# Optimization experiments

Measured on AMD Instinct MI355X. Metric: run time of the kernel, lower is better.

## Reference

```python
import jax, jax.numpy as jnp
from jax import lax
import numpy as np

N_FEATURE = 128
EDGE = 12          # int(sqrt(128) + 1)
BATCH = 131072


def maxpool2(x):
    # 2x2 max pool, stride 2, NCHW
    return lax.reduce_window(x, -jnp.inf, lax.max,
                             (1, 1, 2, 2), (1, 1, 2, 2), 'VALID')


def conv3x3(x, w, b):
    # 3x3 conv, padding=1, NCHW / OIHW
    y = lax.conv_general_dilated(x, w, window_strides=(1, 1),
                                 padding=((1, 1), (1, 1)),
                                 dimension_numbers=('NCHW', 'OIHW', 'NCHW'))
    return y + b[None, :, None, None]


def setup_inputs() -> dict:
    key = jax.random.key(0)
    ks = jax.random.split(key, 9)
    x = jax.random.normal(ks[0], (BATCH, N_FEATURE), dtype=jnp.float32)
    conv1_w = jax.random.normal(ks[1], (3, 1, 3, 3), dtype=jnp.float32) * 0.1
    conv1_b = jnp.zeros((3,), dtype=jnp.float32)
    conv2_w = jax.random.normal(ks[2], (6, 3, 3, 3), dtype=jnp.float32) * 0.1
    conv2_b = jnp.zeros((6,), dtype=jnp.float32)
    fc1_w = jax.random.normal(ks[3], (128, 54), dtype=jnp.float32) * 0.1
    fc1_b = jnp.zeros((128,), dtype=jnp.float32)
    out_w = jax.random.normal(ks[4], (N_FEATURE, 128), dtype=jnp.float32) * 0.1
    out_b = jnp.zeros((N_FEATURE,), dtype=jnp.float32)
    return {"x": x, "conv1_w": conv1_w, "conv1_b": conv1_b,
            "conv2_w": conv2_w, "conv2_b": conv2_b,
            "fc1_w": fc1_w, "fc1_b": fc1_b,
            "out_w": out_w, "out_b": out_b}


def reference(x, conv1_w, conv1_b, conv2_w, conv2_b, fc1_w, fc1_b, out_w, out_b):
    num = x.shape[0]
    n = x.shape[1]                       # 128
    pad = EDGE * EDGE - n                # 16 trailing zeros
    # vectorized transto3D: row-major fill of edge x edge grid, zero-padded tail
    g = jnp.pad(x, ((0, 0), (0, pad))).reshape(num, 1, EDGE, EDGE)
    h = jax.nn.relu(maxpool2(conv3x3(g, conv1_w, conv1_b)))      # [num,3,6,6]
    h = jax.nn.relu(maxpool2(conv3x3(h, conv2_w, conv2_b)))      # [num,6,3,3]
    h = h.reshape(num, 54)
    h = jax.nn.relu(h @ fc1_w.T + fc1_b)                         # [num,128]
    return h @ out_w.T + out_b                                   # [num,128]
```

## Files before the change

### kernel.cpp

```cpp
#include <hip/hip_runtime.h>

typedef unsigned int uint;
typedef unsigned short ushort;

using bf16x8 = __attribute__((ext_vector_type(8))) short;
using f32x4  = __attribute__((ext_vector_type(4))) float;

__device__ __forceinline__ float b2f(ushort u) {
  union { uint i; float f; } v; v.i = ((uint)u) << 16; return v.f;
}
__device__ __forceinline__ ushort f2b(float f) {
  union { float f; uint i; } v; v.f = f;
  uint r = (v.i + 0x7fffu + ((v.i >> 16) & 1u)) >> 16;
  return (ushort)r;
}
__device__ __forceinline__ bf16x8 ldfrag(const ushort* p) {
  union { uint4 u; bf16x8 v; } x; x.u = *(const uint4*)p; return x.v;
}
__device__ __forceinline__ bf16x8 pack8(const float4 a, const float4 b) {
  union { uint4 u; bf16x8 v; } x;
  x.u.x = (uint)f2b(a.x) | ((uint)f2b(a.y) << 16);
  x.u.y = (uint)f2b(a.z) | ((uint)f2b(a.w) << 16);
  x.u.z = (uint)f2b(b.x) | ((uint)f2b(b.y) << 16);
  x.u.w = (uint)f2b(b.z) | ((uint)f2b(b.w) << 16);
  return x.v;
}

__global__ __launch_bounds__(256, 1) void conv_kernel(
    const float* __restrict__ x,
    const float* __restrict__ w1g, const float* __restrict__ b1g,
    const float* __restrict__ w2g, const float* __restrict__ b2g,
    ushort* __restrict__ h2ws) {
  const int s = blockIdx.x * 256 + threadIdx.x;
  const float* xs = x + (size_t)s * 128;

  float xv[128];
#pragma unroll
  for (int i = 0; i < 32; ++i) {
    const float4 v = ((const float4*)xs)[i];
    xv[4 * i + 0] = v.x; xv[4 * i + 1] = v.y;
    xv[4 * i + 2] = v.z; xv[4 * i + 3] = v.w;
  }
#pragma unroll
  for (int i = 0; i < 128; ++i) asm volatile("" : "+v"(xv[i]));

  float w1[3][9], b1[3];
#pragma unroll
  for (int c = 0; c < 3; ++c) {
    b1[c] = b1g[c];
#pragma unroll
    for (int q = 0; q < 9; ++q) w1[c][q] = w1g[c * 9 + q];
  }

  float h1[3][6][6];
#pragma unroll
  for (int pr = 0; pr < 6; ++pr)
#pragma unroll
    for (int pc = 0; pc < 6; ++pc)
#pragma unroll
      for (int ch = 0; ch < 3; ++ch) {
        float m = -3.0e38f;
#pragma unroll
        for (int dr = 0; dr < 2; ++dr)
#pragma unroll
          for (int dc = 0; dc < 2; ++dc) {
            float a = 0.f;
#pragma unroll
            for (int ky = 0; ky < 3; ++ky)
#pragma unroll
              for (int kx = 0; kx < 3; ++kx) {
                const int r = 2 * pr + dr + ky - 1;
                const int c = 2 * pc + dc + kx - 1;
                if (r >= 0 && r < 12 && c >= 0 && c < 12 && (12 * r + c) < 128)
                  a = fmaf(w1[ch][ky * 3 + kx], xv[12 * r + c], a);
              }
            m = fmaxf(m, a);
          }
        h1[ch][pr][pc] = fmaxf(m + b1[ch], 0.f);
      }

  float h2[54];
#pragma unroll
  for (int o = 0; o < 6; ++o) {
    float w2[27];
#pragma unroll
    for (int q = 0; q < 27; ++q) w2[q] = w2g[o * 27 + q];
    const float bo = b2g[o];
#pragma unroll
    for (int qr = 0; qr < 3; ++qr)
#pragma unroll
      for (int qc = 0; qc < 3; ++qc) {
        float m = -3.0e38f;
#pragma unroll
        for (int dr = 0; dr < 2; ++dr)
#pragma unroll
          for (int dc = 0; dc < 2; ++dc) {
            float a = 0.f;
#pragma unroll
            for (int i = 0; i < 3; ++i)
#pragma unroll
              for (int ky = 0; ky < 3; ++ky)
#pragma unroll
                for (int kx = 0; kx < 3; ++kx) {
                  const int yy = 2 * qr + dr + ky - 1;
                  const int xx = 2 * qc + dc + kx - 1;
                  if (yy >= 0 && yy < 6 && xx >= 0 && xx < 6)
                    a = fmaf(w2[i * 9 + ky * 3 + kx], h1[i][yy][xx], a);
                }
            m = fmaxf(m, a);
          }
        h2[o * 9 + qr * 3 + qc] = fmaxf(m + bo, 0.f);
      }
  }

  uint pk[32];
#pragma unroll
  for (int q = 0; q < 27; ++q)
    pk[q] = (uint)f2b(h2[2 * q]) | ((uint)f2b(h2[2 * q + 1]) << 16);
#pragma unroll
  for (int q = 27; q < 32; ++q) pk[q] = 0u;
  uint4* dst = (uint4*)(h2ws + (size_t)s * 64);
#pragma unroll
  for (int i = 0; i < 8; ++i) {
    uint4 v; v.x = pk[4 * i]; v.y = pk[4 * i + 1];
    v.z = pk[4 * i + 2]; v.w = pk[4 * i + 3];
    dst[i] = v;
  }
}

__global__ __launch_bounds__(256, 3) void fc_kernel(
    const ushort* __restrict__ h2ws,
    const float* __restrict__ fc1w, const float* __restrict__ fc1b,
    const float* __restrict__ outw, const float* __restrict__ outb,
    float* __restrict__ out) {
  __shared__ __align__(16) ushort w1s[128][72];
  __shared__ __align__(16) ushort tA[128][132];
  __shared__ __align__(16) float fb1[128];
  __shared__ __align__(16) float ob[128];

  const int t = threadIdx.x;
  const int s0 = blockIdx.x * 128;
  const int lane = t & 63, wv = t >> 6;
  const int quad = lane >> 4, lm = lane & 15;

  bf16x8 bh[2][8];
#pragma unroll
  for (int st = 0; st < 8; ++st) {
    const ushort* rp = h2ws + (size_t)(s0 + 16 * st + lm) * 64 + quad * 8;
    bh[0][st] = ldfrag(rp);
    bh[1][st] = ldfrag(rp + 32);
  }

  if (t < 128) { fb1[t] = fc1b[t]; ob[t] = outb[t]; }

#pragma unroll
  for (int i = 0; i < 27; ++i) {
    const int f = t + 256 * i;
    const int n = f / 54, k = f - 54 * n;
    w1s[n][k] = f2b(fc1w[f]);
  }
  if (t < 128) {
    uint* p = (uint*)&w1s[t][54];
#pragma unroll
    for (int q = 0; q < 5; ++q) p[q] = 0u;
  }
  __syncthreads();

  f32x4 acc[2][8];
#pragma unroll
  for (int mt = 0; mt < 2; ++mt)
#pragma unroll
    for (int st = 0; st < 8; ++st) acc[mt][st] = (f32x4){0.f, 0.f, 0.f, 0.f};

#pragma unroll
  for (int kk = 0; kk < 2; ++kk) {
    const int ko = kk * 32 + quad * 8;
    bf16x8 aw[2];
#pragma unroll
    for (int mt = 0; mt < 2; ++mt)
      aw[mt] = ldfrag(&w1s[32 * wv + 16 * mt + lm][ko]);
#pragma unroll
    for (int mt = 0; mt < 2; ++mt)
#pragma unroll
      for (int st = 0; st < 8; ++st)
        acc[mt][st] = __builtin_amdgcn_mfma_f32_16x16x32_bf16(
            aw[mt], bh[kk][st], acc[mt][st], 0, 0, 0);
  }

#pragma unroll
  for (int mt = 0; mt < 2; ++mt) {
    const int jb = 32 * wv + 16 * mt + quad * 4;
    const float4 bj = *(const float4*)&fb1[jb];
#pragma unroll
    for (int st = 0; st < 8; ++st) {
      const int sR = 16 * st + lm;
      const float v0 = fmaxf(acc[mt][st][0] + bj.x, 0.f);
      const float v1 = fmaxf(acc[mt][st][1] + bj.y, 0.f);
      const float v2 = fmaxf(acc[mt][st][2] + bj.z, 0.f);
      const float v3 = fmaxf(acc[mt][st][3] + bj.w, 0.f);
      uint2 pv;
      pv.x = (uint)f2b(v0) | ((uint)f2b(v1) << 16);
      pv.y = (uint)f2b(v2) | ((uint)f2b(v3) << 16);
      *(uint2*)&tA[sR][jb] = pv;
    }
  }
  __syncthreads();

  f32x4 acc2[2][8];
#pragma unroll
  for (int mt = 0; mt < 2; ++mt)
#pragma unroll
    for (int st = 0; st < 8; ++st) acc2[mt][st] = (f32x4){0.f, 0.f, 0.f, 0.f};

#pragma unroll
  for (int kk = 0; kk < 4; ++kk) {
    const int ko = kk * 32 + quad * 8;
    bf16x8 ao[2], bt[8];
#pragma unroll
    for (int mt = 0; mt < 2; ++mt) {
      const float* rp = outw + (size_t)(32 * wv + 16 * mt + lm) * 128 + ko;
      const float4 v0 = *(const float4*)rp;
      const float4 v1 = *(const float4*)(rp + 4);
      ao[mt] = pack8(v0, v1);
    }
#pragma unroll
    for (int st = 0; st < 8; ++st)
      bt[st] = ldfrag(&tA[16 * st + lm][ko]);
#pragma unroll
    for (int mt = 0; mt < 2; ++mt)
#pragma unroll
      for (int st = 0; st < 8; ++st)
        acc2[mt][st] = __builtin_amdgcn_mfma_f32_16x16x32_bf16(
            ao[mt], bt[st], acc2[mt][st], 0, 0, 0);
  }

#pragma unroll
  for (int mt = 0; mt < 2; ++mt) {
    const int obase = 32 * wv + 16 * mt + quad * 4;
    const float4 b4 = *(const float4*)&ob[obase];
#pragma unroll
    for (int st = 0; st < 8; ++st) {
      const int srow = s0 + 16 * st + lm;
      float4 o4;
      o4.x = acc2[mt][st][0] + b4.x;
      o4.y = acc2[mt][st][1] + b4.y;
      o4.z = acc2[mt][st][2] + b4.z;
      o4.w = acc2[mt][st][3] + b4.w;
      *(float4*)&out[(size_t)srow * 128 + obase] = o4;
    }
  }
}

extern "C" void kernel_launch(void* const* d_in, const int* in_sizes, int n_in,
                              void* d_out, int out_size, void* d_ws, size_t ws_size,
                              hipStream_t stream) {
  const float* x    = (const float*)d_in[0];
  const float* w1   = (const float*)d_in[1];
  const float* b1   = (const float*)d_in[2];
  const float* w2   = (const float*)d_in[3];
  const float* b2   = (const float*)d_in[4];
  const float* fc1w = (const float*)d_in[5];
  const float* fc1b = (const float*)d_in[6];
  const float* outw = (const float*)d_in[7];
  const float* outb = (const float*)d_in[8];
  float* outp = (float*)d_out;
  ushort* ws  = (ushort*)d_ws;

  const int N = in_sizes[0] / 128;

  conv_kernel<<<N / 256, 256, 0, stream>>>(x, w1, b1, w2, b2, ws);
  fc_kernel<<<N / 128, 256, 0, stream>>>(ws, fc1w, fc1b, outw, outb, outp);
}
```

Before: 180.8 us.

## Split conv per sample across three waves by output row band

The conv kernel now gives each sample to three threads, one per pooled conv2 output row. Each thread loads only the input rows it needs and computes only the h1 rows its band requires. Results are staged in shared memory and written to the workspace with coalesced 32-bit stores. This cuts per-thread register pressure and raises occupancy relative to the one-thread-per-sample design at launch bound 1, at the cost of recomputing the overlapping h1 rows and reading some input rows redundantly.

```diff
diff --git a/kernel.cpp b/kernel.cpp
--- a/kernel.cpp
+++ b/kernel.cpp
@@ -26,23 +26,25 @@
   return x.v;
 }
 
-__global__ __launch_bounds__(256, 1) void conv_kernel(
-    const float* __restrict__ x,
+template <int Q>
+__device__ __forceinline__ void conv_sample(
+    const float* __restrict__ xs,
     const float* __restrict__ w1g, const float* __restrict__ b1g,
     const float* __restrict__ w2g, const float* __restrict__ b2g,
-    ushort* __restrict__ h2ws) {
-  const int s = blockIdx.x * 256 + threadIdx.x;
-  const float* xs = x + (size_t)s * 128;
+    ushort* __restrict__ strow) {
+  constexpr int HRLO = (Q == 0) ? 0 : (Q == 1) ? 1 : 3;
+  constexpr int HRHI = (Q == 0) ? 2 : (Q == 1) ? 4 : 5;
+  constexpr int NR = HRHI - HRLO + 1;
+  constexpr int F4LO = (Q == 0) ? 0 : (Q == 1) ? 3 : 15;
+  constexpr int F4HI = (Q == 0) ? 20 : 31;
 
   float xv[128];
 #pragma unroll
-  for (int i = 0; i < 32; ++i) {
+  for (int i = F4LO; i <= F4HI; ++i) {
     const float4 v = ((const float4*)xs)[i];
     xv[4 * i + 0] = v.x; xv[4 * i + 1] = v.y;
     xv[4 * i + 2] = v.z; xv[4 * i + 3] = v.w;
   }
-#pragma unroll
-  for (int i = 0; i < 128; ++i) asm volatile("" : "+v"(xv[i]));
 
   float w1[3][9], b1[3];
 #pragma unroll
@@ -52,9 +54,10 @@
     for (int q = 0; q < 9; ++q) w1[c][q] = w1g[c * 9 + q];
   }
 
-  float h1[3][6][6];
-#pragma unroll
-  for (int pr = 0; pr < 6; ++pr)
+  float h1[3][NR][6];
+#pragma unroll
+  for (int ri = 0; ri < NR; ++ri) {
+    const int hr = HRLO + ri;
 #pragma unroll
     for (int pc = 0; pc < 6; ++pc)
 #pragma unroll
@@ -69,17 +72,17 @@
             for (int ky = 0; ky < 3; ++ky)
 #pragma unroll
               for (int kx = 0; kx < 3; ++kx) {
-                const int r = 2 * pr + dr + ky - 1;
+                const int r = 2 * hr + dr + ky - 1;
                 const int c = 2 * pc + dc + kx - 1;
                 if (r >= 0 && r < 12 && c >= 0 && c < 12 && (12 * r + c) < 128)
                   a = fmaf(w1[ch][ky * 3 + kx], xv[12 * r + c], a);
               }
             m = fmaxf(m, a);
           }
-        h1[ch][pr][pc] = fmaxf(m + b1[ch], 0.f);
+        h1[ch][ri][pc] = fmaxf(m + b1[ch], 0.f);
       }
-
-  float h2[54];
+  }
+
 #pragma unroll
   for (int o = 0; o < 6; ++o) {
     float w2[27];
@@ -87,48 +90,71 @@
     for (int q = 0; q < 27; ++q) w2[q] = w2g[o * 27 + q];
     const float bo = b2g[o];
 #pragma unroll
-    for (int qr = 0; qr < 3; ++qr)
-#pragma unroll
-      for (int qc = 0; qc < 3; ++qc) {
-        float m = -3.0e38f;
-#pragma unroll
-        for (int dr = 0; dr < 2; ++dr)
-#pragma unroll
-          for (int dc = 0; dc < 2; ++dc) {
-            float a = 0.f;
-#pragma unroll
-            for (int i = 0; i < 3; ++i)
-#pragma unroll
-              for (int ky = 0; ky < 3; ++ky)
-#pragma unroll
-                for (int kx = 0; kx < 3; ++kx) {
-                  const int yy = 2 * qr + dr + ky - 1;
-                  const int xx = 2 * qc + dc + kx - 1;
-                  if (yy >= 0 && yy < 6 && xx >= 0 && xx < 6)
-                    a = fmaf(w2[i * 9 + ky * 3 + kx], h1[i][yy][xx], a);
-                }
-            m = fmaxf(m, a);
-          }
-        h2[o * 9 + qr * 3 + qc] = fmaxf(m + bo, 0.f);
-      }
-  }
-
-  uint pk[32];
-#pragma unroll
-  for (int q = 0; q < 27; ++q)
-    pk[q] = (uint)f2b(h2[2 * q]) | ((uint)f2b(h2[2 * q + 1]) << 16);
-#pragma unroll
-  for (int q = 27; q < 32; ++q) pk[q] = 0u;
-  uint4* dst = (uint4*)(h2ws + (size_t)s * 64);
-#pragma unroll
-  for (int i = 0; i < 8; ++i) {
-    uint4 v; v.x = pk[4 * i]; v.y = pk[4 * i + 1];
-    v.z = pk[4 * i + 2]; v.w = pk[4 * i + 3];
-    dst[i] = v;
-  }
-}
-
-__global__ __launch_bounds__(256, 3) void fc_kernel(
+    for (int qc = 0; qc < 3; ++qc) {
+      float m = -3.0e38f;
+#pragma unroll
+      for (int dr = 0; dr < 2; ++dr)
+#pragma unroll
+        for (int dc = 0; dc < 2; ++dc) {
+          float a = 0.f;
+#pragma unroll
+          for (int i = 0; i < 3; ++i)
+#pragma unroll
+            for (int ky = 0; ky < 3; ++ky)
+#pragma unroll
+              for (int kx = 0; kx < 3; ++kx) {
+                const int yy = 2 * Q + dr + ky - 1;
+                const int xx = 2 * qc + dc + kx - 1;
+                if (yy >= HRLO && yy <= HRHI && xx >= 0 && xx < 6)
+                  a = fmaf(w2[i * 9 + ky * 3 + kx], h1[i][yy - HRLO][xx], a);
+              }
+          m = fmaxf(m, a);
+        }
+      strow[o * 9 + Q * 3 + qc] = f2b(fmaxf(m + bo, 0.f));
+    }
+  }
+  if (Q == 2) {
+    uint* p = (uint*)(strow + 54);
+#pragma unroll
+    for (int q = 0; q < 5; ++q) p[q] = 0u;
+  }
+}
+
+__global__ __launch_bounds__(384, 6) void conv_kernel_r7(
+    const float* __restrict__ x,
+    const float* __restrict__ w1g, const float* __restrict__ b1g,
+    const float* __restrict__ w2g, const float* __restrict__ b2g,
+    ushort* __restrict__ h2ws) {
+  __shared__ ushort h2st[128][66];
+
+  const int t = threadIdx.x;
+  const int s0 = blockIdx.x * 128;
+  const int wv = t >> 6;
+  const int q  = (wv < 3) ? wv : wv - 3;
+  const int sg = (wv < 3) ? 0 : 1;
+  const int si = sg * 64 + (t & 63);
+
+  const float* xs = x + (size_t)(s0 + si) * 128;
+  ushort* strow = &h2st[si][0];
+
+  if (q == 0)      conv_sample<0>(xs, w1g, b1g, w2g, b2g, strow);
+  else if (q == 1) conv_sample<1>(xs, w1g, b1g, w2g, b2g, strow);
+  else             conv_sample<2>(xs, w1g, b1g, w2g, b2g, strow);
+
+  __syncthreads();
+
+#pragma unroll
+  for (int i = 0; i < 11; ++i) {
+    const int f = t + 384 * i;
+    if (f < 4096) {
+      const int sr = f >> 5, dw = f & 31;
+      const uint v = *(const uint*)&h2st[sr][dw * 2];
+      ((uint*)h2ws)[((size_t)(s0 + sr) << 5) + dw] = v;
+    }
+  }
+}
+
+__global__ __launch_bounds__(256, 3) void fc_kernel_r7(
     const ushort* __restrict__ h2ws,
     const float* __restrict__ fc1w, const float* __restrict__ fc1b,
     const float* __restrict__ outw, const float* __restrict__ outb,
@@ -268,6 +294,6 @@
 
   const int N = in_sizes[0] / 128;
 
-  conv_kernel<<<N / 256, 256, 0, stream>>>(x, w1, b1, w2, b2, ws);
-  fc_kernel<<<N / 128, 256, 0, stream>>>(ws, fc1w, fc1b, outw, outb, outp);
-}
+  conv_kernel_r7<<<N / 128, 384, 0, stream>>>(x, w1, b1, w2, b2, ws);
+  fc_kernel_r7<<<N / 128, 256, 0, stream>>>(ws, fc1w, fc1b, outw, outb, outp);
+}
```

After: 262.2 us. +45.0%, slower.
